# Kernel tuning notes

Hardware: AMD Instinct MI355X
Metric: run time of the kernel (lower is better)

The kernel has to match this reference:

```python
import jax, jax.numpy as jnp
import numpy as np

N_ITERATIONS = 3
N_OUT_CAPS = 10


def squash(t, axis=-2):
    # squash(s) = ||s||^2 * s / ((1 + ||s||^2) * ||s||)
    sqr_norm = jnp.sum(t * t, axis=axis, keepdims=True)
    norm = jnp.sqrt(sqr_norm)
    return sqr_norm * t / ((1.0 + sqr_norm) * norm)


def setup_inputs() -> dict:
    key = jax.random.key(0)
    B, I, O, D = 256, 1152, 10, 16
    u_hat = jax.random.normal(key, (B, I, O, D, 1), dtype=jnp.float32)
    return {"u_hat": u_hat}


def reference(u_hat):
    B = u_hat.shape[0]
    I, O = u_hat.shape[1], u_hat.shape[2]
    # routing logits b: (B, I, O, 1, 1)
    b = jnp.zeros((B, I, O, 1, 1), dtype=u_hat.dtype)
    v = None
    for r in range(N_ITERATIONS):
        c = jax.nn.softmax(b, axis=1)                 # softmax over input capsules
        s = jnp.sum(c * u_hat, axis=1, keepdims=True)  # (B, 1, O, D, 1)
        v = squash(s, axis=-2)
        if r < N_ITERATIONS - 1:
            # u_hat^T @ v: (B,I,O,1,D) @ (B,1,O,D,1) -> (B,I,O,1,1)
            b = b + jnp.matmul(jnp.swapaxes(u_hat, -2, -1), v)
    return v.reshape(B, N_OUT_CAPS, -1)
```

## Files before the change

kernel.cpp:

```cpp
#include <hip/hip_runtime.h>
#include <math.h>

#define N_I 1152
#define N_O 10
#define N_D 16
#define BLK 256
#define KPT 18
#define ROWS (N_O * N_D)

__device__ __forceinline__ float qadd1(float x) {
    return x + __int_as_float(__builtin_amdgcn_update_dpp(
        0, __float_as_int(x), 0xB1, 0xF, 0xF, true));
}
__device__ __forceinline__ float qadd2(float x) {
    return x + __int_as_float(__builtin_amdgcn_update_dpp(
        0, __float_as_int(x), 0x4E, 0xF, 0xF, true));
}

__global__ __launch_bounds__(BLK, 4)
void caps_route(const float* __restrict__ u_hat, float* __restrict__ out)
{
    __shared__ float4 scr_s[2][4][4];
    __shared__ float  scr_e[2][4];

    const int tid  = threadIdx.x;
    const int wave = tid >> 6;
    const int lane = tid & 63;
    const int d4   = tid & 3;
    const int ig   = tid >> 2;

    const int bid = blockIdx.x;
    const int nwg = gridDim.x;
    int wid = bid;
    if ((nwg & 7) == 0) wid = (bid & 7) * (nwg >> 3) + (bid >> 3);
    const int b = wid / N_O;
    const int o = wid - b * N_O;

    const float* g = u_hat + (size_t)b * (N_I * ROWS) + (size_t)o * N_D
                   + (size_t)ig * ROWS + (size_t)(d4 << 2);

    float4 u[KPT];
    float4 s4 = make_float4(0.f, 0.f, 0.f, 0.f);
    #pragma unroll
    for (int k = 0; k < KPT; ++k) {
        u[k] = *(const float4*)(g + (size_t)(k << 6) * ROWS);
        s4.x += u[k].x; s4.y += u[k].y;
        s4.z += u[k].z; s4.w += u[k].w;
    }
    float esum = (float)KPT;
    float4 vc = make_float4(0.f, 0.f, 0.f, 0.f);
    float4 v4;

    #pragma unroll
    for (int r = 0; r < 3; ++r) {
        if (r > 0) {
            s4 = make_float4(0.f, 0.f, 0.f, 0.f);
            esum = 0.0f;
            #pragma unroll
            for (int k = 0; k < KPT; ++k) {
                float p = u[k].x*vc.x + u[k].y*vc.y + u[k].z*vc.z + u[k].w*vc.w;
                p = qadd1(p);
                p = qadd2(p);
                const float e = __expf(p);
                esum += e;
                s4.x += e*u[k].x; s4.y += e*u[k].y;
                s4.z += e*u[k].z; s4.w += e*u[k].w;
            }
        }
        #pragma unroll
        for (int m = 4; m <= 32; m <<= 1) {
            s4.x += __shfl_xor(s4.x, m);
            s4.y += __shfl_xor(s4.y, m);
            s4.z += __shfl_xor(s4.z, m);
            s4.w += __shfl_xor(s4.w, m);
            esum += __shfl_xor(esum, m);
        }
        const int pp = r & 1;
        if (lane < 4) {
            scr_s[pp][wave][lane] = s4;
            if (lane == 0) scr_e[pp][wave] = esum;
        }
        __syncthreads();
        float4 st = make_float4(0.f, 0.f, 0.f, 0.f);
        float et = 0.f;
        #pragma unroll
        for (int w = 0; w < 4; ++w) {
            const float4 t = scr_s[pp][w][d4];
            st.x += t.x; st.y += t.y; st.z += t.z; st.w += t.w;
            et += scr_e[pp][w];
        }
        const float inv = 1.0f / et;
        st.x *= inv; st.y *= inv; st.z *= inv; st.w *= inv;
        float sq = st.x*st.x + st.y*st.y + st.z*st.z + st.w*st.w;
        sq = qadd1(sq);
        sq = qadd2(sq);
        const float nrm = sqrtf(sq);
        const float f = nrm / (1.0f + sq);
        v4.x = st.x*f; v4.y = st.y*f; v4.z = st.z*f; v4.w = st.w*f;
        if (r < 2) {
            vc.x += v4.x; vc.y += v4.y; vc.z += v4.z; vc.w += v4.w;
        }
    }
    if (tid < 4)
        *(float4*)(out + (size_t)wid * N_D + (tid << 2)) = v4;
}

extern "C" void kernel_launch(void* const* d_in, const int* in_sizes, int n_in,
                              void* d_out, int out_size, void* d_ws, size_t ws_size,
                              hipStream_t stream)
{
    const float* u_hat = (const float*)d_in[0];
    float* out = (float*)d_out;
    const int B = in_sizes[0] / (N_I * N_O * N_D);
    hipLaunchKernelGGL(caps_route, dim3(B * N_O), dim3(BLK), 0, stream, u_hat, out);
}
```

Before: 33.71 us.

## Process five output capsules per block with async global-to-LDS prefetch

Each block now handles five output capsules for one batch element instead of one, launching a fifth as many blocks. The u_hat slice for the next capsule is loaded directly into LDS with global_load_lds while the current capsule's routing runs, so memory latency is meant to overlap with compute. This adds a 72KB LDS buffer, lowers the occupancy hint to 2 blocks, and drops the XCD-aware block remapping. The grid shrinks to 512 blocks, which may leave CUs underused, and the serial loop per block makes each block's run longer.

```diff
diff --git a/kernel.cpp b/kernel.cpp
--- a/kernel.cpp
+++ b/kernel.cpp
@@ -7,6 +7,8 @@
 #define BLK 256
 #define KPT 18
 #define ROWS (N_O * N_D)
+#define NITEM 5
+#define NSLOT (N_I * 4)
 
 __device__ __forceinline__ float qadd1(float x) {
     return x + __int_as_float(__builtin_amdgcn_update_dpp(
@@ -16,10 +18,16 @@
     return x + __int_as_float(__builtin_amdgcn_update_dpp(
         0, __float_as_int(x), 0x4E, 0xF, 0xF, true));
 }
+__device__ __forceinline__ void lgkm_barrier() {
+    asm volatile("s_waitcnt lgkmcnt(0)" ::: "memory");
+    __builtin_amdgcn_s_barrier();
+    __builtin_amdgcn_sched_barrier(0);
+}
 
-__global__ __launch_bounds__(BLK, 4)
+__global__ __launch_bounds__(BLK, 2)
 void caps_route(const float* __restrict__ u_hat, float* __restrict__ out)
 {
+    __shared__ float4 ubuf[NSLOT];
     __shared__ float4 scr_s[2][4][4];
     __shared__ float  scr_e[2][4];
 
@@ -30,79 +38,99 @@
     const int ig   = tid >> 2;
 
     const int bid = blockIdx.x;
-    const int nwg = gridDim.x;
-    int wid = bid;
-    if ((nwg & 7) == 0) wid = (bid & 7) * (nwg >> 3) + (bid >> 3);
-    const int b = wid / N_O;
-    const int o = wid - b * N_O;
+    const int b   = bid >> 1;
+    const int o0  = (bid & 1) * NITEM;
 
-    const float* g = u_hat + (size_t)b * (N_I * ROWS) + (size_t)o * N_D
-                   + (size_t)ig * ROWS + (size_t)(d4 << 2);
+    const float* bbase = u_hat + (size_t)b * (N_I * ROWS) + (size_t)o0 * N_D;
+    float* outb = out + ((size_t)b * N_O + o0) * N_D;
 
-    float4 u[KPT];
-    float4 s4 = make_float4(0.f, 0.f, 0.f, 0.f);
-    #pragma unroll
-    for (int k = 0; k < KPT; ++k) {
-        u[k] = *(const float4*)(g + (size_t)(k << 6) * ROWS);
-        s4.x += u[k].x; s4.y += u[k].y;
-        s4.z += u[k].z; s4.w += u[k].w;
-    }
-    float esum = (float)KPT;
-    float4 vc = make_float4(0.f, 0.f, 0.f, 0.f);
-    float4 v4;
+    auto issue_item = [&](int t) {
+        __builtin_amdgcn_sched_barrier(0);
+        const float* g0 = bbase + t * N_D;
+        #pragma unroll
+        for (int j = 0; j < KPT; ++j) {
+            const int s = j * BLK + tid;
+            const float* g = g0 + (size_t)(s >> 2) * ROWS + (size_t)(s & 3) * 4;
+            float4* dst = ubuf + (j * BLK + (tid & ~63));
+            __builtin_amdgcn_global_load_lds(
+                (const __attribute__((address_space(1))) void*)g,
+                (__attribute__((address_space(3))) void*)dst,
+                16, 0, 0);
+        }
+        __builtin_amdgcn_sched_barrier(0);
+    };
 
-    #pragma unroll
-    for (int r = 0; r < 3; ++r) {
-        if (r > 0) {
-            s4 = make_float4(0.f, 0.f, 0.f, 0.f);
-            esum = 0.0f;
+    issue_item(0);
+
+    for (int t = 0; t < NITEM; ++t) {
+        __syncthreads();
+
+        float4 u[KPT];
+        float4 s4 = make_float4(0.f, 0.f, 0.f, 0.f);
+        #pragma unroll
+        for (int k = 0; k < KPT; ++k) {
+            u[k] = ubuf[((ig + (k << 6)) << 2) | d4];
+            s4.x += u[k].x; s4.y += u[k].y;
+            s4.z += u[k].z; s4.w += u[k].w;
+        }
+        lgkm_barrier();
+        if (t + 1 < NITEM) issue_item(t + 1);
+
+        float esum = (float)KPT;
+        float4 vc = make_float4(0.f, 0.f, 0.f, 0.f);
+        float4 v4;
+        #pragma unroll
+        for (int r = 0; r < 3; ++r) {
+            if (r > 0) {
+                s4 = make_float4(0.f, 0.f, 0.f, 0.f);
+                esum = 0.0f;
+                #pragma unroll
+                for (int k = 0; k < KPT; ++k) {
+                    float p = u[k].x*vc.x + u[k].y*vc.y
+                            + u[k].z*vc.z + u[k].w*vc.w;
+                    p = qadd1(p);
+                    p = qadd2(p);
+                    const float e = __expf(p);
+                    esum += e;
+                    s4.x += e*u[k].x; s4.y += e*u[k].y;
+                    s4.z += e*u[k].z; s4.w += e*u[k].w;
+                }
+            }
             #pragma unroll
-            for (int k = 0; k < KPT; ++k) {
-                float p = u[k].x*vc.x + u[k].y*vc.y + u[k].z*vc.z + u[k].w*vc.w;
-                p = qadd1(p);
-                p = qadd2(p);
-                const float e = __expf(p);
-                esum += e;
-                s4.x += e*u[k].x; s4.y += e*u[k].y;
-                s4.z += e*u[k].z; s4.w += e*u[k].w;
+            for (int m = 4; m <= 32; m <<= 1) {
+                s4.x += __shfl_xor(s4.x, m);
+                s4.y += __shfl_xor(s4.y, m);
+                s4.z += __shfl_xor(s4.z, m);
+                s4.w += __shfl_xor(s4.w, m);
+                esum += __shfl_xor(esum, m);
             }
-        }
-        #pragma unroll
-        for (int m = 4; m <= 32; m <<= 1) {
-            s4.x += __shfl_xor(s4.x, m);
-            s4.y += __shfl_xor(s4.y, m);
-            s4.z += __shfl_xor(s4.z, m);
-            s4.w += __shfl_xor(s4.w, m);
-            esum += __shfl_xor(esum, m);
-        }
-        const int pp = r & 1;
-        if (lane < 4) {
-            scr_s[pp][wave][lane] = s4;
-            if (lane == 0) scr_e[pp][wave] = esum;
-        }
-        __syncthreads();
-        float4 st = make_float4(0.f, 0.f, 0.f, 0.f);
-        float et = 0.f;
-        #pragma unroll
-        for (int w = 0; w < 4; ++w) {
-            const float4 t = scr_s[pp][w][d4];
-            st.x += t.x; st.y += t.y; st.z += t.z; st.w += t.w;
-            et += scr_e[pp][w];
-        }
-        const float inv = 1.0f / et;
-        st.x *= inv; st.y *= inv; st.z *= inv; st.w *= inv;
-        float sq = st.x*st.x + st.y*st.y + st.z*st.z + st.w*st.w;
-        sq = qadd1(sq);
-        sq = qadd2(sq);
-        const float nrm = sqrtf(sq);
-        const float f = nrm / (1.0f + sq);
-        v4.x = st.x*f; v4.y = st.y*f; v4.z = st.z*f; v4.w = st.w*f;
-        if (r < 2) {
+            const int pp = r & 1;
+            if (lane < 4) {
+                scr_s[pp][wave][lane] = s4;
+                if (lane == 0) scr_e[pp][wave] = esum;
+            }
+            lgkm_barrier();
+            float4 st = make_float4(0.f, 0.f, 0.f, 0.f);
+            float et = 0.f;
+            #pragma unroll
+            for (int w = 0; w < 4; ++w) {
+                const float4 q = scr_s[pp][w][d4];
+                st.x += q.x; st.y += q.y; st.z += q.z; st.w += q.w;
+                et += scr_e[pp][w];
+            }
+            const float inv = 1.0f / et;
+            st.x *= inv; st.y *= inv; st.z *= inv; st.w *= inv;
+            float sq = st.x*st.x + st.y*st.y + st.z*st.z + st.w*st.w;
+            sq = qadd1(sq);
+            sq = qadd2(sq);
+            const float nrm = sqrtf(sq);
+            const float f = nrm / (1.0f + sq);
+            v4.x = st.x*f; v4.y = st.y*f; v4.z = st.z*f; v4.w = st.w*f;
             vc.x += v4.x; vc.y += v4.y; vc.z += v4.z; vc.w += v4.w;
         }
+        if (tid < 4)
+            *(float4*)(outb + t * N_D + (tid << 2)) = v4;
     }
-    if (tid < 4)
-        *(float4*)(out + (size_t)wid * N_D + (tid << 2)) = v4;
 }
 
 extern "C" void kernel_launch(void* const* d_in, const int* in_sizes, int n_in,
@@ -112,5 +140,5 @@
     const float* u_hat = (const float*)d_in[0];
     float* out = (float*)d_out;
     const int B = in_sizes[0] / (N_I * N_O * N_D);
-    hipLaunchKernelGGL(caps_route, dim3(B * N_O), dim3(BLK), 0, stream, u_hat, out);
+    hipLaunchKernelGGL(caps_route, dim3(B * 2), dim3(BLK), 0, stream, u_hat, out);
 }
```

New measurement: 63.81 us. 1.89x slower.

## Process two routing items per block with prefetch of next item's data

Applied to the files above, without the earlier changes.

Each block now handles two (batch, out-capsule) items, cutting the grid in half, and issues the global loads for the second item during the last routing iteration of the first. This is meant to hide memory latency behind the first item's reduction and barrier work. It also swaps __expf for exp2f with a pre-scaled vector and replaces __syncthreads with an explicit LDS waitcnt+barrier. In exchange there are half as many blocks to spread across CUs, the block runs twice as long, and the u registers for the second item stay live during the first item's last iteration.

```diff
diff --git a/kernel.cpp b/kernel.cpp
--- a/kernel.cpp
+++ b/kernel.cpp
@@ -7,6 +7,7 @@
 #define BLK 256
 #define KPT 18
 #define ROWS (N_O * N_D)
+#define LOG2E 1.44269504088896340736f
 
 __device__ __forceinline__ float qadd1(float x) {
     return x + __int_as_float(__builtin_amdgcn_update_dpp(
@@ -15,6 +16,98 @@
 __device__ __forceinline__ float qadd2(float x) {
     return x + __int_as_float(__builtin_amdgcn_update_dpp(
         0, __float_as_int(x), 0x4E, 0xF, 0xF, true));
+}
+
+__device__ __forceinline__ void lds_barrier() {
+    asm volatile("s_waitcnt lgkmcnt(0)" ::: "memory");
+    __builtin_amdgcn_s_barrier();
+    __builtin_amdgcn_sched_barrier(0);
+}
+
+__device__ __forceinline__ const float* item_ptr(const float* u_hat, int wid,
+                                                 int ig, int d4)
+{
+    const int b = wid / N_O;
+    const int o = wid - b * N_O;
+    return u_hat + (size_t)b * (N_I * ROWS) + (size_t)o * N_D
+                 + (size_t)ig * ROWS + (size_t)(d4 << 2);
+}
+
+template<bool PRE>
+__device__ __forceinline__ void route_item(
+    float4 (&u)[KPT], const float* __restrict__ gnext,
+    float* __restrict__ outp, int tid, int wave, int lane, int d4, int ppb,
+    float4 (*scr_s)[4][4], float (*scr_e)[4])
+{
+    float4 vc = make_float4(0.f, 0.f, 0.f, 0.f);
+    float4 v4;
+    #pragma unroll
+    for (int r = 0; r < 3; ++r) {
+        float4 s4 = make_float4(0.f, 0.f, 0.f, 0.f);
+        float esum;
+        if (r == 0) {
+            #pragma unroll
+            for (int k = 0; k < KPT; ++k) {
+                s4.x += u[k].x; s4.y += u[k].y;
+                s4.z += u[k].z; s4.w += u[k].w;
+            }
+            esum = (float)KPT;
+        } else {
+            esum = 0.f;
+            const float4 vl = make_float4(vc.x*LOG2E, vc.y*LOG2E,
+                                          vc.z*LOG2E, vc.w*LOG2E);
+            #pragma unroll
+            for (int k = 0; k < KPT; ++k) {
+                float p = u[k].x*vl.x + u[k].y*vl.y + u[k].z*vl.z + u[k].w*vl.w;
+                p = qadd1(p);
+                p = qadd2(p);
+                const float e = exp2f(p);
+                esum += e;
+                s4.x += e*u[k].x; s4.y += e*u[k].y;
+                s4.z += e*u[k].z; s4.w += e*u[k].w;
+            }
+        }
+        if (PRE && r == 2) {
+            __builtin_amdgcn_sched_barrier(0);
+            #pragma unroll
+            for (int k = 0; k < KPT; ++k)
+                u[k] = *(const float4*)(gnext + (size_t)(k << 6) * ROWS);
+            __builtin_amdgcn_sched_barrier(0);
+        }
+        #pragma unroll
+        for (int m = 4; m <= 32; m <<= 1) {
+            s4.x += __shfl_xor(s4.x, m);
+            s4.y += __shfl_xor(s4.y, m);
+            s4.z += __shfl_xor(s4.z, m);
+            s4.w += __shfl_xor(s4.w, m);
+            esum += __shfl_xor(esum, m);
+        }
+        const int pp = (ppb + r) & 1;
+        if (lane < 4) {
+            scr_s[pp][wave][lane] = s4;
+            if (lane == 0) scr_e[pp][wave] = esum;
+        }
+        lds_barrier();
+        float4 st = make_float4(0.f, 0.f, 0.f, 0.f);
+        float et = 0.f;
+        #pragma unroll
+        for (int w = 0; w < 4; ++w) {
+            const float4 q = scr_s[pp][w][d4];
+            st.x += q.x; st.y += q.y; st.z += q.z; st.w += q.w;
+            et += scr_e[pp][w];
+        }
+        const float inv = 1.0f / et;
+        st.x *= inv; st.y *= inv; st.z *= inv; st.w *= inv;
+        float sq = st.x*st.x + st.y*st.y + st.z*st.z + st.w*st.w;
+        sq = qadd1(sq);
+        sq = qadd2(sq);
+        const float nrm = sqrtf(sq);
+        const float f = nrm / (1.0f + sq);
+        v4.x = st.x*f; v4.y = st.y*f; v4.z = st.z*f; v4.w = st.w*f;
+        vc.x += v4.x; vc.y += v4.y; vc.z += v4.z; vc.w += v4.w;
+    }
+    if (tid < 4)
+        *(float4*)(outp + (tid << 2)) = v4;
 }
 
 __global__ __launch_bounds__(BLK, 4)
@@ -31,78 +124,23 @@
 
     const int bid = blockIdx.x;
     const int nwg = gridDim.x;
-    int wid = bid;
-    if ((nwg & 7) == 0) wid = (bid & 7) * (nwg >> 3) + (bid >> 3);
-    const int b = wid / N_O;
-    const int o = wid - b * N_O;
+    int slot = bid;
+    if ((nwg & 7) == 0) slot = (bid & 7) * (nwg >> 3) + (bid >> 3);
+    const int wid0 = slot;
+    const int wid1 = slot + nwg;
 
-    const float* g = u_hat + (size_t)b * (N_I * ROWS) + (size_t)o * N_D
-                   + (size_t)ig * ROWS + (size_t)(d4 << 2);
+    const float* g0 = item_ptr(u_hat, wid0, ig, d4);
+    const float* g1 = item_ptr(u_hat, wid1, ig, d4);
 
     float4 u[KPT];
-    float4 s4 = make_float4(0.f, 0.f, 0.f, 0.f);
     #pragma unroll
-    for (int k = 0; k < KPT; ++k) {
-        u[k] = *(const float4*)(g + (size_t)(k << 6) * ROWS);
-        s4.x += u[k].x; s4.y += u[k].y;
-        s4.z += u[k].z; s4.w += u[k].w;
-    }
-    float esum = (float)KPT;
-    float4 vc = make_float4(0.f, 0.f, 0.f, 0.f);
-    float4 v4;
+    for (int k = 0; k < KPT; ++k)
+        u[k] = *(const float4*)(g0 + (size_t)(k << 6) * ROWS);
 
-    #pragma unroll
-    for (int r = 0; r < 3; ++r) {
-        if (r > 0) {
-            s4 = make_float4(0.f, 0.f, 0.f, 0.f);
-            esum = 0.0f;
-            #pragma unroll
-            for (int k = 0; k < KPT; ++k) {
-                float p = u[k].x*vc.x + u[k].y*vc.y + u[k].z*vc.z + u[k].w*vc.w;
-                p = qadd1(p);
-                p = qadd2(p);
-                const float e = __expf(p);
-                esum += e;
-                s4.x += e*u[k].x; s4.y += e*u[k].y;
-                s4.z += e*u[k].z; s4.w += e*u[k].w;
-            }
-        }
-        #pragma unroll
-        for (int m = 4; m <= 32; m <<= 1) {
-            s4.x += __shfl_xor(s4.x, m);
-            s4.y += __shfl_xor(s4.y, m);
-            s4.z += __shfl_xor(s4.z, m);
-            s4.w += __shfl_xor(s4.w, m);
-            esum += __shfl_xor(esum, m);
-        }
-        const int pp = r & 1;
-        if (lane < 4) {
-            scr_s[pp][wave][lane] = s4;
-            if (lane == 0) scr_e[pp][wave] = esum;
-        }
-        __syncthreads();
-        float4 st = make_float4(0.f, 0.f, 0.f, 0.f);
-        float et = 0.f;
-        #pragma unroll
-        for (int w = 0; w < 4; ++w) {
-            const float4 t = scr_s[pp][w][d4];
-            st.x += t.x; st.y += t.y; st.z += t.z; st.w += t.w;
-            et += scr_e[pp][w];
-        }
-        const float inv = 1.0f / et;
-        st.x *= inv; st.y *= inv; st.z *= inv; st.w *= inv;
-        float sq = st.x*st.x + st.y*st.y + st.z*st.z + st.w*st.w;
-        sq = qadd1(sq);
-        sq = qadd2(sq);
-        const float nrm = sqrtf(sq);
-        const float f = nrm / (1.0f + sq);
-        v4.x = st.x*f; v4.y = st.y*f; v4.z = st.z*f; v4.w = st.w*f;
-        if (r < 2) {
-            vc.x += v4.x; vc.y += v4.y; vc.z += v4.z; vc.w += v4.w;
-        }
-    }
-    if (tid < 4)
-        *(float4*)(out + (size_t)wid * N_D + (tid << 2)) = v4;
+    route_item<true >(u, g1, out + (size_t)wid0 * N_D,
+                      tid, wave, lane, d4, 0, scr_s, scr_e);
+    route_item<false>(u, (const float*)0, out + (size_t)wid1 * N_D,
+                      tid, wave, lane, d4, 3, scr_s, scr_e);
 }
 
 extern "C" void kernel_launch(void* const* d_in, const int* in_sizes, int n_in,
@@ -112,5 +150,6 @@
     const float* u_hat = (const float*)d_in[0];
     float* out = (float*)d_out;
     const int B = in_sizes[0] / (N_I * N_O * N_D);
-    hipLaunchKernelGGL(caps_route, dim3(B * N_O), dim3(BLK), 0, stream, u_hat, out);
+    hipLaunchKernelGGL(caps_route, dim3(B * N_O / 2), dim3(BLK), 0, stream,
+                       u_hat, out);
 }
```

Result: slower. 41.06 us (+21.8%).
